# Kernel tuning notes

Measured on AMD Instinct MI355X. Metric: run time of the kernel, lower is better.

## Reference

```python
import jax, jax.numpy as jnp
import numpy as np

H, D, VD = 8, 64, 64
QD, KD, VDIM, OUT = 512, 512, 512, 512
N, QS, VS = 16, 512, 512
TEMP = 10.0              # softstair_temp
SCALING = D ** -0.5


def _softstair(x):
    fl = jnp.floor(x)
    return fl + jax.nn.sigmoid(TEMP * (jnp.abs(x - fl) - 0.5))


def setup_inputs() -> dict:
    key = jax.random.key(0)
    ks = jax.random.split(key, 24)
    f = jax.random.normal
    s = 0.03  # xavier-ish scale
    return {
        "Q": f(ks[0], (N, QS, QD), jnp.float32),
        "K": f(ks[1], (N, VS, KD), jnp.float32),
        "V": f(ks[2], (N, VS, VDIM), jnp.float32),
        "past_state": f(ks[3], (N, H, QS, D), jnp.float32),
        "past_attention": jax.random.uniform(ks[4], (N, H, QS, 1), jnp.float32),
        "value_positions": jnp.arange(VS, dtype=jnp.float32),
        "attention_mask": jnp.ones((N, QS, VS), jnp.int32),
        "Wq": f(ks[5], (QD, H * D), jnp.float32) * s,
        "Wk": f(ks[6], (KD, H * D), jnp.float32) * s,
        "Wv": f(ks[7], (VDIM, H * VD), jnp.float32) * s,
        "Wpos": f(ks[8], (QD, H * D), jnp.float32) * s,
        "bpos": f(ks[9], (H * D,), jnp.float32) * s,
        "Wsigma": f(ks[10], (H, D, 1), jnp.float32) * s,
        "Wrho": f(ks[11], (H, D, 3), jnp.float32) * s,
        "mix_w": f(ks[12], (QD, 1), jnp.float32) * s,
        "mix_b": f(ks[13], (1,), jnp.float32) * s,
        "gru_wi": f(ks[14], (D, 3 * D), jnp.float32) * s,
        "gru_wh": f(ks[15], (D, 3 * D), jnp.float32) * s,
        "gru_bi": f(ks[16], (3 * D,), jnp.float32) * s,
        "gru_bh": f(ks[17], (3 * D,), jnp.float32) * s,
        "Wc": f(ks[18], (H * VD, OUT), jnp.float32) * s,
    }


def reference(Q, K, V, past_state, past_attention, value_positions, attention_mask,
              Wq, Wk, Wv, Wpos, bpos, Wsigma, Wrho, mix_w, mix_b,
              gru_wi, gru_wh, gru_bi, gru_bh, Wc):
    n, qS, _ = Q.shape
    vS = K.shape[1]
    mask_f = attention_mask.astype(jnp.float32)          # [N,qS,vS]
    mask_b = attention_mask.astype(bool)[:, None]        # [N,1,qS,vS]
    lengths = jnp.sum(mask_f, axis=-1)                   # [N,qS]
    l_1 = jnp.maximum(1.0, lengths - 1.0)[:, None, :, None]
    step_size = 1.0 / l_1                                # [N,1,qS,1]
    nvp = value_positions[None, None, None, :] * step_size  # [N,1,qS,vS]

    # mix gate
    mix = jax.nn.sigmoid(Q @ mix_w + mix_b)[:, None]     # [N,1,qS,1]

    # projections -> [N,H,S,d]
    Qpos = (Q @ Wpos + bpos).reshape(n, qS, H, D).transpose(0, 2, 1, 3)
    Qh = (Q @ Wq).reshape(n, qS, H, D).transpose(0, 2, 1, 3)
    Kh = (K @ Wk).reshape(n, vS, H, D).transpose(0, 2, 1, 3)
    Vh = (V @ Wv).reshape(n, vS, H, VD).transpose(0, 2, 1, 3)

    # content attention
    content = jnp.einsum('bhqd,bhkd->bhqk', Qh, Kh) * SCALING
    content_attn = jax.nn.softmax(jnp.where(mask_b, content, -jnp.inf), axis=-1)

    # GRUCell update (torch gate order r,z,n) on relu(Qpos) with past_state
    x = jax.nn.relu(Qpos)
    gi = x @ gru_wi + gru_bi
    gh = past_state @ gru_wh + gru_bh
    ir, iz, inn = jnp.split(gi, 3, axis=-1)
    hr, hz, hn = jnp.split(gh, 3, axis=-1)
    r = jax.nn.sigmoid(ir + hr)
    z = jax.nn.sigmoid(iz + hz)
    nn_ = jnp.tanh(inn + r * hn)
    state = (1.0 - z) * nn_ + z * past_state             # [N,H,qS,D]

    # location (Gaussian) attention
    sigma = (jax.nn.relu(jnp.einsum('bhqd,hde->bhqe', state, Wsigma)) + 0.27) \
            / lengths[:, None, :, None]                  # [N,H,qS,1]
    rho = jnp.einsum('bhqd,hde->bhqe', state, Wrho)      # [N,H,qS,3]
    steps = _softstair(rho[..., 0:1])
    attn_gate = jax.nn.sigmoid(rho[..., 1:2])
    bias_gate = jax.nn.sigmoid(rho[..., 2:3])
    mu_ = steps * step_size + attn_gate * past_attention + bias_gate
    # leaky clamp to [0,1]
    mu = jnp.maximum(0.01 * mu_, jnp.minimum(mu_, 1.0 + 0.01 * mu_))
    diff = nvp - mu                                      # [N,H,qS,vS]
    gauss = jnp.exp(-(diff * diff) / (2.0 * sigma * sigma))
    g = gauss * mask_f[:, None]
    pos_attn = g / jnp.sum(g + 1e-20, axis=-1, keepdims=True)

    scores = mix * pos_attn + (1.0 - mix) * content_attn
    attended = jnp.einsum('bhqk,bhkv->bhqv', scores, Vh)
    out = attended.transpose(0, 2, 1, 3).reshape(n, qS, H * VD) @ Wc
    return out
```

## Files before the change

kernel.cpp:

```cpp
#include <hip/hip_runtime.h>


typedef __bf16 bf16;
typedef __bf16 bfx8 __attribute__((ext_vector_type(8)));
typedef float v4f __attribute__((ext_vector_type(4)));

__device__ inline float sigm(float x) { return 1.0f / (1.0f + __expf(-x)); }
__device__ inline float tanh_fast(float x) { return 1.0f - 2.0f / (__expf(2.0f * x) + 1.0f); }

__device__ inline v4f mfma16(bfx8 a, bfx8 b, v4f c) {
    return __builtin_amdgcn_mfma_f32_16x16x32_bf16(a, b, c, 0, 0, 0);
}

typedef const __attribute__((address_space(1))) void* gvp;
typedef __attribute__((address_space(3))) void* lvp;

__device__ inline void gload_lds16(const bf16* g, bf16* l) {
    __builtin_amdgcn_global_load_lds((gvp)g, (lvp)l, 16, 0, 0);
}

__device__ inline void split8(const float* __restrict__ p, bfx8& hi, bfx8& lo) {
    float4 x = *(const float4*)p;
    float4 y = *(const float4*)(p + 4);
    float v[8] = {x.x, x.y, x.z, x.w, y.x, y.y, y.z, y.w};
#pragma unroll
    for (int j = 0; j < 8; ++j) {
        bf16 h = (bf16)v[j];
        hi[j] = h;
        lo[j] = (bf16)(v[j] - (float)h);
    }
}

struct PrepArgs {
    const float* wsrc[5]; bf16* wdst[5]; bf16* wdstlo[5];
    const float* gwi; const float* gwh;
    bf16* wih; bf16* wil; bf16* whh; bf16* whl;
    const float* Q; const int* mask; const float* mix_w; const float* mix_b;
    float* mixv; float* stepv; float* lenv; unsigned* mpack;
};

__global__ __launch_bounds__(256) void prep_kernel(PrepArgs a) {
    __shared__ __align__(16) char smraw[17408];
    const int b = blockIdx.x;
    const int t = threadIdx.x;

    if (b < 320) {
        float (*tile)[68] = (float(*)[68])smraw;
        const int wy = b >> 6, bx = b & 63;
        const float* src = a.wsrc[wy];
        bf16* dst = a.wdst[wy];
        bf16* dlo = a.wdstlo[wy];
        const int rbase = (bx >> 3) * 64, cbase = (bx & 7) * 64;
        const int r = t >> 2, cc = (t & 3) * 16;
        {
            const float* p = src + (long)(rbase + r) * 512 + cbase + cc;
            *(float4*)(&tile[r][cc]) = *(const float4*)p;
            *(float4*)(&tile[r][cc + 4]) = *(const float4*)(p + 4);
            *(float4*)(&tile[r][cc + 8]) = *(const float4*)(p + 8);
            *(float4*)(&tile[r][cc + 12]) = *(const float4*)(p + 12);
        }
        __syncthreads();
        bfx8 h0, h1, l0, l1;
#pragma unroll
        for (int j = 0; j < 8; ++j) {
            float v0 = tile[cc + j][r];
            float v1 = tile[cc + 8 + j][r];
            bf16 a0 = (bf16)v0, a1 = (bf16)v1;
            h0[j] = a0; l0[j] = (bf16)(v0 - (float)a0);
            h1[j] = a1; l1[j] = (bf16)(v1 - (float)a1);
        }
        const int n_ = cbase + r;
        const int x_ = (n_ & 7) << 3;
        const long rowo = (long)n_ * 512;
        const int ka = (rbase + cc) ^ x_;
        const int kb = (rbase + cc + 8) ^ x_;
        *(bfx8*)(dst + rowo + ka) = h0;
        *(bfx8*)(dst + rowo + kb) = h1;
        if (dlo) {
            *(bfx8*)(dlo + rowo + ka) = l0;
            *(bfx8*)(dlo + rowo + kb) = l1;
        }
        return;
    }

    if (b < 322) {
        const int m = b - 320;
        const float* src = m ? a.gwh : a.gwi;
        bf16* dh = m ? a.whh : a.wih;
        bf16* dl = m ? a.whl : a.wil;
        for (int e = t; e < 12288; e += 256) {
            int row = e >> 7, col = e & 127;
            int cc = col >> 3, j = col & 7;
            int nt = row >> 3, ks = (row >> 2) & 1, quad = row & 3;
            int k = ks * 32 + quad * 8 + j;
            float v = src[k * 192 + nt * 16 + cc];
            bf16 h = (bf16)v;
            dh[e] = h;
            dl[e] = (bf16)(v - (float)h);
        }
        return;
    }

    unsigned (*mwords)[16] = (unsigned(*)[16])smraw;
    const int bm = b - 322;
    const int qt = bm & 31, n = bm >> 5;
    const int wave = t >> 6, lane = t & 63;
#pragma unroll
    for (int rr = 0; rr < 4; ++rr) {
        const int rloc = wave * 4 + rr;
        const long row = (long)n * 512 + qt * 16 + rloc;
        float dot = 0.f, ms = 0.f;
        unsigned myw = 0;
#pragma unroll
        for (int j = 0; j < 8; ++j) {
            float qv = a.Q[row * 512 + j * 64 + lane];
            float wv = a.mix_w[j * 64 + lane];
            dot += qv * wv;
            int mv = a.mask[row * 512 + j * 64 + lane];
            unsigned long long bl = __ballot(mv != 0);
            ms += (float)__popcll(bl);
            if ((lane >> 1) == j) myw = (unsigned)(bl >> ((lane & 1) * 32));
        }
#pragma unroll
        for (int o = 32; o > 0; o >>= 1) dot += __shfl_xor(dot, o);
        if (lane < 16) mwords[rloc][lane] = myw;
        if (lane == 0) {
            a.mixv[row] = sigm(dot + a.mix_b[0]);
            a.lenv[row] = ms;
            a.stepv[row] = 1.0f / fmaxf(1.0f, ms - 1.0f);
        }
    }
    __syncthreads();
    {
        const int quad = (lane >> 4), c = lane & 15;
        unsigned out = 0;
#pragma unroll
        for (int i = 0; i < 4; ++i) {
            const int rl = quad * 4 + i;
            unsigned w0 = mwords[rl][wave * 4 + 0];
            unsigned w1 = mwords[rl][wave * 4 + 1];
            unsigned w2 = mwords[rl][wave * 4 + 2];
            unsigned w3 = mwords[rl][wave * 4 + 3];
            unsigned byte_ = ((w0 >> c) & 1u) | (((w0 >> (16 + c)) & 1u) << 1) |
                             (((w1 >> c) & 1u) << 2) | (((w1 >> (16 + c)) & 1u) << 3) |
                             (((w2 >> c) & 1u) << 4) | (((w2 >> (16 + c)) & 1u) << 5) |
                             (((w3 >> c) & 1u) << 6) | (((w3 >> (16 + c)) & 1u) << 7);
            out |= byte_ << (8 * i);
        }
        a.mpack[(long)bm * 256 + t] = out;
    }
}

struct GEMMDesc {
    const float* Af;
    const bf16* Ab;
    const bf16* B0;
    const bf16* B1;
    const float* bias;
    bf16* Cb;
    bf16* Cl;
    float* Cf;
    int mode;
    float cscale;
};
struct G4 { GEMMDesc d[4]; };

__global__ __launch_bounds__(256, 2) void gemm128(G4 gg) {
    __shared__ bf16 sm[32768];

    const GEMMDesc g = gg.d[blockIdx.z];
    const int mode = g.mode;
    const int mbase = blockIdx.x * 128, nbase = blockIdx.y * 128;
    const int t = threadIdx.x, w = t >> 6, l = t & 63;
    const int quad = l >> 4, c = l & 15;
    const int wr = w >> 1, wc = w & 1;

    const v4f zero4 = {0.f, 0.f, 0.f, 0.f};
    v4f acc[4][4];
#pragma unroll
    for (int m = 0; m < 4; ++m)
#pragma unroll
        for (int nn = 0; nn < 4; ++nn) acc[m][nn] = zero4;

    const int nsteps = (mode == 2) ? 24 : 8;
    const int arow_t = t >> 3;
    const int ach = t & 7;
    const int asw = ((ach ^ (arow_t & 7)) * 8);
    const int xm = c & 7;
    const int slot0 = w * 4;
    const int srow = l >> 3;
    const int sch8 = (l & 7) * 8;

    float4 ax[4], ay[4];

    auto issue = [&](int s, bf16* As, bf16* Bs) {
        const bf16* Bsrc = g.B0;
        int k0;
        if (mode == 2) {
            int ph = s >> 3;
            k0 = (s & 7) * 64;
            if (ph == 1) Bsrc = g.B1;
        } else {
            k0 = s * 64;
        }
#pragma unroll
        for (int j = 0; j < 4; ++j) {
            int sl = slot0 + j;
            int row = sl * 8 + srow;
            gload_lds16(Bsrc + (long)(nbase + row) * 512 + k0 + sch8, Bs + sl * 512);
        }
        if (mode == 3) {
#pragma unroll
            for (int j = 0; j < 4; ++j) {
                int sl = slot0 + j;
                int row = sl * 8 + srow;
                gload_lds16(g.Ab + (long)(mbase + row) * 512 + k0 + sch8, As + sl * 512);
            }
        } else {
#pragma unroll
            for (int j = 0; j < 4; ++j) {
                const float* p = g.Af + (long)(mbase + j * 32 + arow_t) * 512 + k0 + ach * 8;
                ax[j] = *(const float4*)p;
                ay[j] = *(const float4*)(p + 4);
            }
        }
    };

    auto writeA = [&](int s, bf16* As) {
        if (mode == 3) return;
        const bool lo = (mode == 2) && ((s >> 3) == 2);
#pragma unroll
        for (int j = 0; j < 4; ++j) {
            float v[8] = {ax[j].x, ax[j].y, ax[j].z, ax[j].w,
                          ay[j].x, ay[j].y, ay[j].z, ay[j].w};
            bfx8 hv;
            if (!lo) {
#pragma unroll
                for (int q = 0; q < 8; ++q) hv[q] = (bf16)v[q];
            } else {
#pragma unroll
                for (int q = 0; q < 8; ++q) {
                    bf16 h = (bf16)v[q];
                    hv[q] = (bf16)(v[q] - (float)h);
                }
            }
            *(bfx8*)(&As[(j * 32 + arow_t) * 64 + asw]) = hv;
        }
    };

    auto compute = [&](const bf16* As, const bf16* Bs) {
#pragma unroll
        for (int ks = 0; ks < 2; ++ks) {
            const int off = (((ks * 4 + quad) ^ xm) * 8);
            bfx8 af[4], bb[4];
#pragma unroll
            for (int m = 0; m < 4; ++m)
                af[m] = *(const bfx8*)(&As[(wr * 64 + m * 16 + c) * 64 + off]);
#pragma unroll
            for (int nn = 0; nn < 4; ++nn)
                bb[nn] = *(const bfx8*)(&Bs[(wc * 64 + nn * 16 + c) * 64 + off]);
#pragma unroll
            for (int m = 0; m < 4; ++m)
#pragma unroll
                for (int nn = 0; nn < 4; ++nn)
                    acc[m][nn] = mfma16(af[m], bb[nn], acc[m][nn]);
        }
    };

    issue(0, sm, sm + 8192);
    writeA(0, sm);
    __syncthreads();
    for (int s = 0; s < nsteps; ++s) {
        bf16* Ac = sm + (s & 1) * 16384;
        bf16* An = sm + (((s & 1) ^ 1) * 16384);
        const bool more = (s + 1 < nsteps);
        if (more) issue(s + 1, An, An + 8192);
        compute(Ac, Ac + 8192);
        if (more) writeA(s + 1, An);
        __syncthreads();
    }

    if (mode == 3) {
        float* C = g.Cf;
#pragma unroll
        for (int m = 0; m < 4; ++m)
#pragma unroll
            for (int nn = 0; nn < 4; ++nn)
#pragma unroll
                for (int i = 0; i < 4; ++i) {
                    int row = mbase + wr * 64 + m * 16 + quad * 4 + i;
                    int col = nbase + wc * 64 + nn * 16 + c;
                    C[(long)row * 512 + col] = acc[m][nn][i];
                }
        return;
    }

    if (mode == 1) {
        bf16* CT = g.Cb + ((long)(mbase >> 9)) * 262144;
        const int s0 = mbase & 511;
        for (int h = 0; h < 2; ++h) {
            if (wr == h) {
#pragma unroll
                for (int m = 0; m < 4; ++m)
#pragma unroll
                    for (int nn = 0; nn < 4; ++nn)
#pragma unroll
                        for (int i = 0; i < 4; ++i)
                            sm[(wc * 64 + nn * 16 + c) * 64 + m * 16 + quad * 4 + i] =
                                (bf16)acc[m][nn][i];
            }
            __syncthreads();
            {
                const bf16* src = sm + (t >> 1) * 64 + (t & 1) * 32;
                bf16* d = CT + (long)(nbase + (t >> 1)) * 512 + s0 + h * 64 + (t & 1) * 32;
#pragma unroll
                for (int j = 0; j < 4; ++j) *(bfx8*)(d + j * 8) = *(const bfx8*)(src + j * 8);
            }
            __syncthreads();
        }
        return;
    }

    for (int h = 0; h < 2; ++h) {
        if (wr == h) {
#pragma unroll
            for (int m = 0; m < 4; ++m)
#pragma unroll
                for (int nn = 0; nn < 4; ++nn)
#pragma unroll
                    for (int i = 0; i < 4; ++i) {
                        int col = wc * 64 + nn * 16 + c;
                        float v = acc[m][nn][i];
                        if (mode == 2) v = fmaxf(v + g.bias[nbase + col], 0.f);
                        else v *= g.cscale;
                        bf16 hv = (bf16)v;
                        sm[(m * 16 + quad * 4 + i) * 128 + col] = hv;
                        if (mode == 2)
                            sm[8192 + (m * 16 + quad * 4 + i) * 128 + col] =
                                (bf16)(v - (float)hv);
                    }
        }
        __syncthreads();
        {
            const int row = t >> 2, seg = t & 3;
            const bf16* src = sm + row * 128 + seg * 32;
            bf16* d = g.Cb + (long)(mbase + h * 64 + row) * 512 + nbase + seg * 32;
#pragma unroll
            for (int j = 0; j < 4; ++j) *(bfx8*)(d + j * 8) = *(const bfx8*)(src + j * 8);
            if (mode == 2) {
                const bf16* src2 = sm + 8192 + row * 128 + seg * 32;
                bf16* d2 = g.Cl + (long)(mbase + h * 64 + row) * 512 + nbase + seg * 32;
#pragma unroll
                for (int j = 0; j < 4; ++j) *(bfx8*)(d2 + j * 8) = *(const bfx8*)(src2 + j * 8);
            }
        }
        __syncthreads();
    }
}

__global__ __launch_bounds__(256) void gru_fused_kernel(
    const bf16* __restrict__ Xh, const bf16* __restrict__ Xl,
    const float* __restrict__ hp,
    const bf16* __restrict__ wih, const bf16* __restrict__ wil,
    const bf16* __restrict__ whh, const bf16* __restrict__ whl,
    const float* __restrict__ gbi, const float* __restrict__ gbh,
    const float* __restrict__ pa, const float* __restrict__ Wsigma,
    const float* __restrict__ Wrho,
    const float* __restrict__ lenv, const float* __restrict__ stepv,
    float* __restrict__ muv, float* __restrict__ sigv) {
    const int b = blockIdx.x;
    const int qb = b & 7, nh = b >> 3, hd = nh & 7, n = nh >> 3;
    const int t = threadIdx.x;
    const int w = t >> 6, lane = t & 63, quad = lane >> 4, c = lane & 15;
    const int q0 = qb * 64 + w * 16;
    const int fbase = quad * 128 + c * 8;

    const v4f zero4 = {0.f, 0.f, 0.f, 0.f};
    v4f gi[12], gh[12];
#pragma unroll
    for (int nt = 0; nt < 12; ++nt) gi[nt] = zero4;
#pragma unroll
    for (int ks = 0; ks < 2; ++ks) {
        long ao = (long)(n * 512 + q0 + c) * 512 + hd * 64 + ks * 32 + quad * 8;
        bfx8 xh = *(const bfx8*)(Xh + ao);
        bfx8 xl = *(const bfx8*)(Xl + ao);
#pragma unroll
        for (int nt = 0; nt < 12; ++nt) {
            const int fo = (nt * 2 + ks) * 512 + fbase;
            bfx8 bh = *(const bfx8*)(wih + fo);
            bfx8 bl = *(const bfx8*)(wil + fo);
            gi[nt] = mfma16(xh, bh, gi[nt]);
            gi[nt] = mfma16(xh, bl, gi[nt]);
            gi[nt] = mfma16(xl, bh, gi[nt]);
        }
    }
#pragma unroll
    for (int nt = 0; nt < 12; ++nt) gh[nt] = zero4;
#pragma unroll
    for (int ks = 0; ks < 2; ++ks) {
        bfx8 ah, al;
        split8(hp + (long)(nh * 512 + q0 + c) * 64 + ks * 32 + quad * 8, ah, al);
#pragma unroll
        for (int nt = 0; nt < 12; ++nt) {
            const int fo = (nt * 2 + ks) * 512 + fbase;
            bfx8 bh = *(const bfx8*)(whh + fo);
            bfx8 bl = *(const bfx8*)(whl + fo);
            gh[nt] = mfma16(ah, bh, gh[nt]);
            gh[nt] = mfma16(ah, bl, gh[nt]);
            gh[nt] = mfma16(al, bh, gh[nt]);
        }
    }

    float st[4][4];
#pragma unroll
    for (int t4 = 0; t4 < 4; ++t4) {
        float bir = gbi[t4 * 16 + c];
        float biz = gbi[64 + t4 * 16 + c];
        float bin = gbi[128 + t4 * 16 + c];
        float bhr = gbh[t4 * 16 + c];
        float bhz = gbh[64 + t4 * 16 + c];
        float bhn = gbh[128 + t4 * 16 + c];
#pragma unroll
        for (int i = 0; i < 4; ++i) {
            int row = q0 + quad * 4 + i;
            float r = sigm(gi[t4][i] + bir + gh[t4][i] + bhr);
            float z = sigm(gi[t4 + 4][i] + biz + gh[t4 + 4][i] + bhz);
            float nn_ = tanh_fast(gi[t4 + 8][i] + bin + r * (gh[t4 + 8][i] + bhn));
            float hpv = hp[(long)(nh * 512 + row) * 64 + t4 * 16 + c];
            st[t4][i] = (1.0f - z) * nn_ + z * hpv;
        }
    }

    float ws_[4], wr0[4], wr1[4], wr2[4];
#pragma unroll
    for (int t4 = 0; t4 < 4; ++t4) {
        int d = t4 * 16 + c;
        ws_[t4] = Wsigma[hd * 64 + d];
        wr0[t4] = Wrho[(hd * 64 + d) * 3 + 0];
        wr1[t4] = Wrho[(hd * 64 + d) * 3 + 1];
        wr2[t4] = Wrho[(hd * 64 + d) * 3 + 2];
    }
#pragma unroll
    for (int i = 0; i < 4; ++i) {
        float s0 = 0.f, s1 = 0.f, s2 = 0.f, s3 = 0.f;
#pragma unroll
        for (int t4 = 0; t4 < 4; ++t4) {
            float sv = st[t4][i];
            s0 += sv * ws_[t4];
            s1 += sv * wr0[t4];
            s2 += sv * wr1[t4];
            s3 += sv * wr2[t4];
        }
#pragma unroll
        for (int o = 1; o < 16; o <<= 1) {
            s0 += __shfl_xor(s0, o);
            s1 += __shfl_xor(s1, o);
            s2 += __shfl_xor(s2, o);
            s3 += __shfl_xor(s3, o);
        }
        if (c == 0) {
            int row = q0 + quad * 4 + i;
            int idx = nh * 512 + row, rq = n * 512 + row;
            float L = lenv[rq], sp = stepv[rq];
            float sg = (fmaxf(s0, 0.f) + 0.27f) / L;
            float fl = floorf(s1);
            float steps = fl + sigm(10.0f * (fabsf(s1 - fl) - 0.5f));
            float ag = sigm(s2), bg = sigm(s3);
            float mu_ = steps * sp + ag * pa[idx] + bg;
            float mu = fmaxf(0.01f * mu_, fminf(mu_, 1.0f + 0.01f * mu_));
            muv[idx] = mu;
            sigv[idx] = sg;
        }
    }
}

__global__ __launch_bounds__(256) void attn_fused_kernel(
    const bf16* __restrict__ Qh, const bf16* __restrict__ Kh,
    const bf16* __restrict__ VhT, const unsigned* __restrict__ mpack,
    const float* __restrict__ vpos, const float* __restrict__ mixv,
    const float* __restrict__ stepv, const float* __restrict__ muv,
    const float* __restrict__ sigv, bf16* __restrict__ att) {
    __shared__ bf16 Pp[16][520];
    __shared__ bf16 Pg[16][520];

    const int b = blockIdx.x;
    const int nh = ((b >> 8) << 3) | (b & 7);
    const int qt = (b >> 3) & 31;
    const int hd = nh & 7, n = nh >> 3;
    const int t = threadIdx.x;
    const int wave = t >> 6, lane = t & 63;
    const int quad = lane >> 4, c = lane & 15;
    const int qloc = quad * 4;

    const bf16* qrow = Qh + (long)(n * 512 + qt * 16 + c) * 512 + hd * 64 + quad * 8;
    bfx8 afr0 = *(const bfx8*)qrow;
    bfx8 afr1 = *(const bfx8*)(qrow + 32);

    const v4f zero4 = {0.f, 0.f, 0.f, 0.f};
    v4f acc[8];
#pragma unroll
    for (int i = 0; i < 8; ++i) acc[i] = zero4;

    const bf16* kbase = Kh + (long)(n * 512 + wave * 128 + c) * 512 + hd * 64 + quad * 8;
#pragma unroll
    for (int t8 = 0; t8 < 8; ++t8) {
        bfx8 b0 = *(const bfx8*)(kbase + (long)t8 * 16 * 512);
        bfx8 b1 = *(const bfx8*)(kbase + (long)t8 * 16 * 512 + 32);
        acc[t8] = mfma16(afr0, b0, acc[t8]);
        acc[t8] = mfma16(afr1, b1, acc[t8]);
    }

    float mu_[4], c2n[4], stp[4];
#pragma unroll
    for (int i = 0; i < 4; ++i) {
        int q = qt * 16 + qloc + i;
        int idx = nh * 512 + q, rq = n * 512 + q;
        mu_[i] = muv[idx];
        float sg = sigv[idx];
        c2n[i] = -0.72134752f / (sg * sg);
        stp[i] = stepv[rq];
    }

    const unsigned mb32 = mpack[(long)(n * 32 + qt) * 256 + t];
    unsigned mbits[4];
#pragma unroll
    for (int i = 0; i < 4; ++i) mbits[i] = (mb32 >> (8 * i)) & 0xffu;

    float vp[8];
#pragma unroll
    for (int t8 = 0; t8 < 8; ++t8) vp[t8] = vpos[wave * 128 + t8 * 16 + c];

#pragma unroll
    for (int i = 0; i < 4; ++i) {
        float m = mu_[i], s = stp[i], cg = c2n[i];
#pragma unroll
        for (int t8 = 0; t8 < 8; ++t8) {
            int on = (mbits[i] >> t8) & 1;
            float pv = on ? __builtin_amdgcn_exp2f(acc[t8][i]) : 0.f;
            float d = vp[t8] * s - m;
            float gv = on ? __builtin_amdgcn_exp2f(d * d * cg) : 0.f;
            int k = wave * 128 + t8 * 16 + c;
            Pp[qloc + i][k] = (bf16)pv;
            Pg[qloc + i][k] = (bf16)gv;
        }
    }

    __syncthreads();

    bfx8 ones;
#pragma unroll
    for (int j = 0; j < 8; ++j) ones[j] = (bf16)1.0f;

    v4f accP = zero4, accG = zero4, accS = zero4, accT = zero4;
    const bf16* vrow = VhT + (long)(n * 512 + hd * 64 + wave * 16 + c) * 512 + quad * 8;
    __builtin_amdgcn_s_setprio(1);
#pragma unroll
    for (int ks = 0; ks < 16; ++ks) {
        bfx8 bf_ = *(const bfx8*)(vrow + ks * 32);
        bfx8 ap = *(const bfx8*)(&Pp[c][ks * 32 + quad * 8]);
        bfx8 ag = *(const bfx8*)(&Pg[c][ks * 32 + quad * 8]);
        accP = mfma16(ap, bf_, accP);
        accG = mfma16(ag, bf_, accG);
        accS = mfma16(ap, ones, accS);
        accT = mfma16(ag, ones, accT);
    }
    __builtin_amdgcn_s_setprio(0);

#pragma unroll
    for (int i = 0; i < 4; ++i) {
        float Sp = accS[i];
        float Sg = accT[i] + 512.0f * 1e-20f;
        float m_ = mixv[n * 512 + qt * 16 + qloc + i];
        float aci = (1.0f - m_) / Sp;
        float bci = m_ / Sg;
        int q = qt * 16 + quad * 4 + i;
        int cx = (wave * 16 + c) ^ (((quad * 4 + i) & 7) << 3);
        att[(long)(n * 512 + q) * 512 + hd * 64 + cx] =
            (bf16)(aci * accP[i] + bci * accG[i]);
    }
}

extern "C" void kernel_launch(void* const* d_in, const int* in_sizes, int n_in,
                              void* d_out, int out_size, void* d_ws, size_t ws_size,
                              hipStream_t stream) {
    (void)in_sizes; (void)n_in; (void)out_size; (void)ws_size;

    const float* Q = (const float*)d_in[0];
    const float* K = (const float*)d_in[1];
    const float* V = (const float*)d_in[2];
    const float* past_state = (const float*)d_in[3];
    const float* past_att = (const float*)d_in[4];
    const float* vpos = (const float*)d_in[5];
    const int* mask = (const int*)d_in[6];
    const float* Wq = (const float*)d_in[7];
    const float* Wk = (const float*)d_in[8];
    const float* Wv = (const float*)d_in[9];
    const float* Wpos = (const float*)d_in[10];
    const float* bpos = (const float*)d_in[11];
    const float* Wsigma = (const float*)d_in[12];
    const float* Wrho = (const float*)d_in[13];
    const float* mix_w = (const float*)d_in[14];
    const float* mix_b = (const float*)d_in[15];
    const float* gwi = (const float*)d_in[16];
    const float* gwh = (const float*)d_in[17];
    const float* gbi = (const float*)d_in[18];
    const float* gbh = (const float*)d_in[19];
    const float* Wc = (const float*)d_in[20];
    float* out = (float*)d_out;

    char* p = (char*)d_ws;
    const size_t SZB = 8192UL * 512 * 2;
    const size_t SZW = 512UL * 512 * 2;
    bf16* WqT = (bf16*)p;   p += SZW;
    bf16* WkT = (bf16*)p;   p += SZW;
    bf16* WvT = (bf16*)p;   p += SZW;
    bf16* WpT = (bf16*)p;   p += SZW;
    bf16* WpTl = (bf16*)p;  p += SZW;
    bf16* WcT = (bf16*)p;   p += SZW;
    bf16* wih = (bf16*)p;   p += 24576;
    bf16* wil = (bf16*)p;   p += 24576;
    bf16* whh = (bf16*)p;   p += 24576;
    bf16* whl = (bf16*)p;   p += 24576;
    bf16* Qh = (bf16*)p;    p += SZB;
    bf16* Kh = (bf16*)p;    p += SZB;
    bf16* VhT = (bf16*)p;   p += SZB;
    bf16* Xh = (bf16*)p;
    bf16* att = Xh;         p += SZB;
    bf16* Xl = (bf16*)p;    p += SZB;
    unsigned* mpack = (unsigned*)p;      p += 16UL * 32 * 256 * 4;
    float* mixv = (float*)p;  p += 32768;
    float* stepv = (float*)p; p += 32768;
    float* lenv = (float*)p;  p += 32768;
    float* muv = (float*)p;   p += 262144;
    float* sigv = (float*)p;  p += 262144;

    dim3 blk(256);

    PrepArgs pa;
    pa.wsrc[0] = Wq; pa.wsrc[1] = Wk; pa.wsrc[2] = Wv; pa.wsrc[3] = Wpos; pa.wsrc[4] = Wc;
    pa.wdst[0] = WqT; pa.wdst[1] = WkT; pa.wdst[2] = WvT; pa.wdst[3] = WpT; pa.wdst[4] = WcT;
    pa.wdstlo[0] = nullptr; pa.wdstlo[1] = nullptr; pa.wdstlo[2] = nullptr;
    pa.wdstlo[3] = WpTl; pa.wdstlo[4] = nullptr;
    pa.gwi = gwi; pa.gwh = gwh;
    pa.wih = wih; pa.wil = wil; pa.whh = whh; pa.whl = whl;
    pa.Q = Q; pa.mask = mask; pa.mix_w = mix_w; pa.mix_b = mix_b;
    pa.mixv = mixv; pa.stepv = stepv; pa.lenv = lenv; pa.mpack = mpack;
    prep_kernel<<<dim3(834), blk, 0, stream>>>(pa);

    G4 gp;
    gp.d[0].Af = Q;  gp.d[0].Ab = nullptr; gp.d[0].B0 = WpT; gp.d[0].B1 = WpTl;
    gp.d[0].bias = bpos; gp.d[0].Cb = Xh; gp.d[0].Cl = Xl; gp.d[0].Cf = nullptr;
    gp.d[0].mode = 2; gp.d[0].cscale = 1.0f;
    gp.d[1].Af = Q;  gp.d[1].Ab = nullptr; gp.d[1].B0 = WqT; gp.d[1].B1 = nullptr;
    gp.d[1].bias = nullptr; gp.d[1].Cb = Qh; gp.d[1].Cl = nullptr; gp.d[1].Cf = nullptr;
    gp.d[1].mode = 0; gp.d[1].cscale = 0.125f * 1.44269504089f;
    gp.d[2].Af = K;  gp.d[2].Ab = nullptr; gp.d[2].B0 = WkT; gp.d[2].B1 = nullptr;
    gp.d[2].bias = nullptr; gp.d[2].Cb = Kh; gp.d[2].Cl = nullptr; gp.d[2].Cf = nullptr;
    gp.d[2].mode = 0; gp.d[2].cscale = 1.0f;
    gp.d[3].Af = V;  gp.d[3].Ab = nullptr; gp.d[3].B0 = WvT; gp.d[3].B1 = nullptr;
    gp.d[3].bias = nullptr; gp.d[3].Cb = VhT; gp.d[3].Cl = nullptr; gp.d[3].Cf = nullptr;
    gp.d[3].mode = 1; gp.d[3].cscale = 1.0f;
    gemm128<<<dim3(64, 4, 4), blk, 0, stream>>>(gp);

    gru_fused_kernel<<<dim3(1024), blk, 0, stream>>>(
        Xh, Xl, past_state, wih, wil, whh, whl, gbi, gbh, past_att, Wsigma, Wrho,
        lenv, stepv, muv, sigv);

    attn_fused_kernel<<<dim3(4096), blk, 0, stream>>>(
        Qh, Kh, VhT, mpack, vpos, mixv, stepv, muv, sigv, att);

    G4 go;
    go.d[0].Af = nullptr; go.d[0].Ab = att; go.d[0].B0 = WcT; go.d[0].B1 = nullptr;
    go.d[0].bias = nullptr; go.d[0].Cb = nullptr; go.d[0].Cl = nullptr; go.d[0].Cf = out;
    go.d[0].mode = 3; go.d[0].cscale = 1.0f;
    go.d[1] = go.d[0]; go.d[2] = go.d[0]; go.d[3] = go.d[0];
    gemm128<<<dim3(64, 4, 1), blk, 0, stream>>>(go);
}
```

Before: 338.3 us.

## Pre-convert Q/K/V to bf16 in prep and load GEMM A operands directly to registers

The prep kernel gains extra blocks that convert Q, K and V from fp32 to bf16, plus a low-order split of Q, into new workspace buffers. The projection GEMM then reads A fragments straight from global memory into registers instead of staging converted fp32 through LDS, which halves shared memory and raises launch bounds to 3 blocks per SU. The GRU kernel stages its weights and biases in LDS with a plain row layout, and the attention output drops its XOR swizzle. The cost is an extra full pass over Q/K/V in memory and uncoalesced register loads of A, in exchange for less LDS traffic and higher occupancy in the GEMM.

```diff
diff --git a/kernel.cpp b/kernel.cpp
--- a/kernel.cpp
+++ b/kernel.cpp
@@ -37,6 +37,8 @@
     bf16* wih; bf16* wil; bf16* whh; bf16* whl;
     const float* Q; const int* mask; const float* mix_w; const float* mix_b;
     float* mixv; float* stepv; float* lenv; unsigned* mpack;
+    const float* Kf; const float* Vf;
+    bf16* Qbf; bf16* Qlo; bf16* Kbf; bf16* Vbf;
 };
 
 __global__ __launch_bounds__(256) void prep_kernel(PrepArgs a) {
@@ -89,11 +91,8 @@
         bf16* dh = m ? a.whh : a.wih;
         bf16* dl = m ? a.whl : a.wil;
         for (int e = t; e < 12288; e += 256) {
-            int row = e >> 7, col = e & 127;
-            int cc = col >> 3, j = col & 7;
-            int nt = row >> 3, ks = (row >> 2) & 1, quad = row & 3;
-            int k = ks * 32 + quad * 8 + j;
-            float v = src[k * 192 + nt * 16 + cc];
+            int n_ = e >> 6, k = e & 63;
+            float v = src[k * 192 + n_];
             bf16 h = (bf16)v;
             dh[e] = h;
             dl[e] = (bf16)(v - (float)h);
@@ -101,59 +100,86 @@
         return;
     }
 
-    unsigned (*mwords)[16] = (unsigned(*)[16])smraw;
-    const int bm = b - 322;
-    const int qt = bm & 31, n = bm >> 5;
-    const int wave = t >> 6, lane = t & 63;
-#pragma unroll
-    for (int rr = 0; rr < 4; ++rr) {
-        const int rloc = wave * 4 + rr;
-        const long row = (long)n * 512 + qt * 16 + rloc;
-        float dot = 0.f, ms = 0.f;
-        unsigned myw = 0;
-#pragma unroll
-        for (int j = 0; j < 8; ++j) {
-            float qv = a.Q[row * 512 + j * 64 + lane];
-            float wv = a.mix_w[j * 64 + lane];
-            dot += qv * wv;
-            int mv = a.mask[row * 512 + j * 64 + lane];
-            unsigned long long bl = __ballot(mv != 0);
-            ms += (float)__popcll(bl);
-            if ((lane >> 1) == j) myw = (unsigned)(bl >> ((lane & 1) * 32));
-        }
-#pragma unroll
-        for (int o = 32; o > 0; o >>= 1) dot += __shfl_xor(dot, o);
-        if (lane < 16) mwords[rloc][lane] = myw;
-        if (lane == 0) {
-            a.mixv[row] = sigm(dot + a.mix_b[0]);
-            a.lenv[row] = ms;
-            a.stepv[row] = 1.0f / fmaxf(1.0f, ms - 1.0f);
-        }
-    }
-    __syncthreads();
-    {
-        const int quad = (lane >> 4), c = lane & 15;
-        unsigned out = 0;
-#pragma unroll
-        for (int i = 0; i < 4; ++i) {
-            const int rl = quad * 4 + i;
-            unsigned w0 = mwords[rl][wave * 4 + 0];
-            unsigned w1 = mwords[rl][wave * 4 + 1];
-            unsigned w2 = mwords[rl][wave * 4 + 2];
-            unsigned w3 = mwords[rl][wave * 4 + 3];
-            unsigned byte_ = ((w0 >> c) & 1u) | (((w0 >> (16 + c)) & 1u) << 1) |
-                             (((w1 >> c) & 1u) << 2) | (((w1 >> (16 + c)) & 1u) << 3) |
-                             (((w2 >> c) & 1u) << 4) | (((w2 >> (16 + c)) & 1u) << 5) |
-                             (((w3 >> c) & 1u) << 6) | (((w3 >> (16 + c)) & 1u) << 7);
-            out |= byte_ << (8 * i);
-        }
-        a.mpack[(long)bm * 256 + t] = out;
+    if (b < 834) {
+        unsigned (*mwords)[16] = (unsigned(*)[16])smraw;
+        const int bm = b - 322;
+        const int qt = bm & 31, n = bm >> 5;
+        const int wave = t >> 6, lane = t & 63;
+#pragma unroll
+        for (int rr = 0; rr < 4; ++rr) {
+            const int rloc = wave * 4 + rr;
+            const long row = (long)n * 512 + qt * 16 + rloc;
+            float dot = 0.f, ms = 0.f;
+            unsigned myw = 0;
+#pragma unroll
+            for (int j = 0; j < 8; ++j) {
+                float qv = a.Q[row * 512 + j * 64 + lane];
+                float wv = a.mix_w[j * 64 + lane];
+                dot += qv * wv;
+                int mv = a.mask[row * 512 + j * 64 + lane];
+                unsigned long long bl = __ballot(mv != 0);
+                ms += (float)__popcll(bl);
+                if ((lane >> 1) == j) myw = (unsigned)(bl >> ((lane & 1) * 32));
+            }
+#pragma unroll
+            for (int o = 32; o > 0; o >>= 1) dot += __shfl_xor(dot, o);
+            if (lane < 16) mwords[rloc][lane] = myw;
+            if (lane == 0) {
+                a.mixv[row] = sigm(dot + a.mix_b[0]);
+                a.lenv[row] = ms;
+                a.stepv[row] = 1.0f / fmaxf(1.0f, ms - 1.0f);
+            }
+        }
+        __syncthreads();
+        {
+            const int quad = (lane >> 4), c = lane & 15;
+            unsigned out = 0;
+#pragma unroll
+            for (int i = 0; i < 4; ++i) {
+                const int rl = quad * 4 + i;
+                unsigned w0 = mwords[rl][wave * 4 + 0];
+                unsigned w1 = mwords[rl][wave * 4 + 1];
+                unsigned w2 = mwords[rl][wave * 4 + 2];
+                unsigned w3 = mwords[rl][wave * 4 + 3];
+                unsigned byte_ = ((w0 >> c) & 1u) | (((w0 >> (16 + c)) & 1u) << 1) |
+                                 (((w1 >> c) & 1u) << 2) | (((w1 >> (16 + c)) & 1u) << 3) |
+                                 (((w2 >> c) & 1u) << 4) | (((w2 >> (16 + c)) & 1u) << 5) |
+                                 (((w3 >> c) & 1u) << 6) | (((w3 >> (16 + c)) & 1u) << 7);
+                out |= byte_ << (8 * i);
+            }
+            a.mpack[(long)bm * 256 + t] = out;
+        }
+        return;
+    }
+
+    const int cb = b - 834;
+    const int tensor = cb >> 10;
+    const long off = ((long)(cb & 1023) * 256 + t) * 16;
+    const float* s_ = tensor == 0 ? a.Q : (tensor == 1 ? a.Kf : a.Vf);
+    const float4* sp = (const float4*)(s_ + off);
+    float4 x0 = sp[0], x1 = sp[1], x2 = sp[2], x3 = sp[3];
+    float v[16] = {x0.x, x0.y, x0.z, x0.w, x1.x, x1.y, x1.z, x1.w,
+                   x2.x, x2.y, x2.z, x2.w, x3.x, x3.y, x3.z, x3.w};
+    bfx8 h0, h1, l0, l1;
+#pragma unroll
+    for (int j = 0; j < 8; ++j) {
+        bf16 ha = (bf16)v[j], hb = (bf16)v[8 + j];
+        h0[j] = ha; h1[j] = hb;
+        l0[j] = (bf16)(v[j] - (float)ha);
+        l1[j] = (bf16)(v[8 + j] - (float)hb);
+    }
+    bf16* dh = tensor == 0 ? a.Qbf : (tensor == 1 ? a.Kbf : a.Vbf);
+    *(bfx8*)(dh + off) = h0;
+    *(bfx8*)(dh + off + 8) = h1;
+    if (tensor == 0) {
+        *(bfx8*)(a.Qlo + off) = l0;
+        *(bfx8*)(a.Qlo + off + 8) = l1;
     }
 }
 
 struct GEMMDesc {
-    const float* Af;
-    const bf16* Ab;
+    const bf16* A0;
+    const bf16* A1;
     const bf16* B0;
     const bf16* B1;
     const float* bias;
@@ -165,8 +191,10 @@
 };
 struct G4 { GEMMDesc d[4]; };
 
-__global__ __launch_bounds__(256, 2) void gemm128(G4 gg) {
-    __shared__ bf16 sm[32768];
+__global__ __launch_bounds__(256, 3) void gemm128(G4 gg) {
+    __shared__ bf16 sm[16384];
+    bf16* Bs0 = sm;
+    bf16* Bs1 = sm + 8192;
 
     const GEMMDesc g = gg.d[blockIdx.z];
     const int mode = g.mode;
@@ -183,79 +211,39 @@
         for (int nn = 0; nn < 4; ++nn) acc[m][nn] = zero4;
 
     const int nsteps = (mode == 2) ? 24 : 8;
-    const int arow_t = t >> 3;
-    const int ach = t & 7;
-    const int asw = ((ach ^ (arow_t & 7)) * 8);
     const int xm = c & 7;
     const int slot0 = w * 4;
     const int srow = l >> 3;
     const int sch8 = (l & 7) * 8;
-
-    float4 ax[4], ay[4];
-
-    auto issue = [&](int s, bf16* As, bf16* Bs) {
-        const bf16* Bsrc = g.B0;
-        int k0;
-        if (mode == 2) {
-            int ph = s >> 3;
-            k0 = (s & 7) * 64;
-            if (ph == 1) Bsrc = g.B1;
-        } else {
-            k0 = s * 64;
-        }
+    const long arow = (long)(mbase + wr * 64 + c) * 512 + quad * 8;
+
+    auto issueB = [&](int s, bf16* Bs) {
+        const bf16* Bsrc = (mode == 2 && ((s >> 3) == 1)) ? g.B1 : g.B0;
+        const int k0 = (mode == 2) ? (s & 7) * 64 : s * 64;
 #pragma unroll
         for (int j = 0; j < 4; ++j) {
             int sl = slot0 + j;
             int row = sl * 8 + srow;
             gload_lds16(Bsrc + (long)(nbase + row) * 512 + k0 + sch8, Bs + sl * 512);
         }
-        if (mode == 3) {
-#pragma unroll
-            for (int j = 0; j < 4; ++j) {
-                int sl = slot0 + j;
-                int row = sl * 8 + srow;
-                gload_lds16(g.Ab + (long)(mbase + row) * 512 + k0 + sch8, As + sl * 512);
-            }
-        } else {
-#pragma unroll
-            for (int j = 0; j < 4; ++j) {
-                const float* p = g.Af + (long)(mbase + j * 32 + arow_t) * 512 + k0 + ach * 8;
-                ax[j] = *(const float4*)p;
-                ay[j] = *(const float4*)(p + 4);
-            }
-        }
     };
 
-    auto writeA = [&](int s, bf16* As) {
-        if (mode == 3) return;
-        const bool lo = (mode == 2) && ((s >> 3) == 2);
-#pragma unroll
-        for (int j = 0; j < 4; ++j) {
-            float v[8] = {ax[j].x, ax[j].y, ax[j].z, ax[j].w,
-                          ay[j].x, ay[j].y, ay[j].z, ay[j].w};
-            bfx8 hv;
-            if (!lo) {
-#pragma unroll
-                for (int q = 0; q < 8; ++q) hv[q] = (bf16)v[q];
-            } else {
-#pragma unroll
-                for (int q = 0; q < 8; ++q) {
-                    bf16 h = (bf16)v[q];
-                    hv[q] = (bf16)(v[q] - (float)h);
-                }
-            }
-            *(bfx8*)(&As[(j * 32 + arow_t) * 64 + asw]) = hv;
+    auto loadA = [&](int s, bfx8 (&dst)[8]) {
+        const bf16* Asrc = (mode == 2 && ((s >> 3) == 2)) ? g.A1 : g.A0;
+        const int k0 = (mode == 2) ? (s & 7) * 64 : s * 64;
+#pragma unroll
+        for (int m = 0; m < 4; ++m) {
+            const bf16* pr = Asrc + arow + (long)m * 16 * 512 + k0;
+            dst[m * 2 + 0] = *(const bfx8*)pr;
+            dst[m * 2 + 1] = *(const bfx8*)(pr + 32);
         }
     };
 
-    auto compute = [&](const bf16* As, const bf16* Bs) {
+    auto computeB = [&](const bf16* Bs, const bfx8 (&af)[8]) {
 #pragma unroll
         for (int ks = 0; ks < 2; ++ks) {
             const int off = (((ks * 4 + quad) ^ xm) * 8);
-            bfx8 af[4], bb[4];
-#pragma unroll
-            for (int m = 0; m < 4; ++m)
-                af[m] = *(const bfx8*)(&As[(wr * 64 + m * 16 + c) * 64 + off]);
+            bfx8 bb[4];
 #pragma unroll
             for (int nn = 0; nn < 4; ++nn)
                 bb[nn] = *(const bfx8*)(&Bs[(wc * 64 + nn * 16 + c) * 64 + off]);
@@ -263,20 +251,25 @@
             for (int m = 0; m < 4; ++m)
 #pragma unroll
                 for (int nn = 0; nn < 4; ++nn)
-                    acc[m][nn] = mfma16(af[m], bb[nn], acc[m][nn]);
+                    acc[m][nn] = mfma16(af[m * 2 + ks], bb[nn], acc[m][nn]);
         }
     };
 
-    issue(0, sm, sm + 8192);
-    writeA(0, sm);
+    bfx8 aA[8], aB[8];
+    issueB(0, Bs0);
+    loadA(0, aA);
     __syncthreads();
-    for (int s = 0; s < nsteps; ++s) {
-        bf16* Ac = sm + (s & 1) * 16384;
-        bf16* An = sm + (((s & 1) ^ 1) * 16384);
-        const bool more = (s + 1 < nsteps);
-        if (more) issue(s + 1, An, An + 8192);
-        compute(Ac, Ac + 8192);
-        if (more) writeA(s + 1, An);
+    for (int s = 0; s < nsteps; s += 2) {
+        issueB(s + 1, Bs1);
+        loadA(s + 1, aB);
+        computeB(Bs0, aA);
+        __syncthreads();
+        const bool more = (s + 2 < nsteps);
+        if (more) {
+            issueB(s + 2, Bs0);
+            loadA(s + 2, aA);
+        }
+        computeB(Bs1, aB);
         __syncthreads();
     }
 
@@ -368,12 +361,24 @@
     const float* __restrict__ Wrho,
     const float* __restrict__ lenv, const float* __restrict__ stepv,
     float* __restrict__ muv, float* __restrict__ sigv) {
+    __shared__ bf16 Wh[192][72], Wl[192][72];
+    __shared__ float biL[384];
+
     const int b = blockIdx.x;
     const int qb = b & 7, nh = b >> 3, hd = nh & 7, n = nh >> 3;
     const int t = threadIdx.x;
     const int w = t >> 6, lane = t & 63, quad = lane >> 4, c = lane & 15;
     const int q0 = qb * 64 + w * 16;
-    const int fbase = quad * 128 + c * 8;
+
+    if (t < 192) { biL[t] = gbi[t]; biL[192 + t] = gbh[t]; }
+#pragma unroll
+    for (int it = 0; it < 6; ++it) {
+        int task = it * 256 + t;
+        int r = task >> 3, ch = task & 7;
+        *(bfx8*)(&Wh[r][ch * 8]) = *(const bfx8*)(wih + r * 64 + ch * 8);
+        *(bfx8*)(&Wl[r][ch * 8]) = *(const bfx8*)(wil + r * 64 + ch * 8);
+    }
+    __syncthreads();
 
     const v4f zero4 = {0.f, 0.f, 0.f, 0.f};
     v4f gi[12], gh[12];
@@ -386,14 +391,22 @@
         bfx8 xl = *(const bfx8*)(Xl + ao);
 #pragma unroll
         for (int nt = 0; nt < 12; ++nt) {
-            const int fo = (nt * 2 + ks) * 512 + fbase;
-            bfx8 bh = *(const bfx8*)(wih + fo);
-            bfx8 bl = *(const bfx8*)(wil + fo);
+            bfx8 bh = *(const bfx8*)(&Wh[nt * 16 + c][ks * 32 + quad * 8]);
+            bfx8 bl = *(const bfx8*)(&Wl[nt * 16 + c][ks * 32 + quad * 8]);
             gi[nt] = mfma16(xh, bh, gi[nt]);
             gi[nt] = mfma16(xh, bl, gi[nt]);
             gi[nt] = mfma16(xl, bh, gi[nt]);
         }
     }
+    __syncthreads();
+#pragma unroll
+    for (int it = 0; it < 6; ++it) {
+        int task = it * 256 + t;
+        int r = task >> 3, ch = task & 7;
+        *(bfx8*)(&Wh[r][ch * 8]) = *(const bfx8*)(whh + r * 64 + ch * 8);
+        *(bfx8*)(&Wl[r][ch * 8]) = *(const bfx8*)(whl + r * 64 + ch * 8);
+    }
+    __syncthreads();
 #pragma unroll
     for (int nt = 0; nt < 12; ++nt) gh[nt] = zero4;
 #pragma unroll
@@ -402,9 +415,8 @@
         split8(hp + (long)(nh * 512 + q0 + c) * 64 + ks * 32 + quad * 8, ah, al);
 #pragma unroll
         for (int nt = 0; nt < 12; ++nt) {
-            const int fo = (nt * 2 + ks) * 512 + fbase;
-            bfx8 bh = *(const bfx8*)(whh + fo);
-            bfx8 bl = *(const bfx8*)(whl + fo);
+            bfx8 bh = *(const bfx8*)(&Wh[nt * 16 + c][ks * 32 + quad * 8]);
+            bfx8 bl = *(const bfx8*)(&Wl[nt * 16 + c][ks * 32 + quad * 8]);
             gh[nt] = mfma16(ah, bh, gh[nt]);
             gh[nt] = mfma16(ah, bl, gh[nt]);
             gh[nt] = mfma16(al, bh, gh[nt]);
@@ -414,12 +426,12 @@
     float st[4][4];
 #pragma unroll
     for (int t4 = 0; t4 < 4; ++t4) {
-        float bir = gbi[t4 * 16 + c];
-        float biz = gbi[64 + t4 * 16 + c];
-        float bin = gbi[128 + t4 * 16 + c];
-        float bhr = gbh[t4 * 16 + c];
-        float bhz = gbh[64 + t4 * 16 + c];
-        float bhn = gbh[128 + t4 * 16 + c];
+        float bir = biL[t4 * 16 + c];
+        float biz = biL[64 + t4 * 16 + c];
+        float bin = biL[128 + t4 * 16 + c];
+        float bhr = biL[192 + t4 * 16 + c];
+        float bhz = biL[256 + t4 * 16 + c];
+        float bhn = biL[320 + t4 * 16 + c];
 #pragma unroll
         for (int i = 0; i < 4; ++i) {
             int row = q0 + quad * 4 + i;
@@ -574,8 +586,7 @@
         float aci = (1.0f - m_) / Sp;
         float bci = m_ / Sg;
         int q = qt * 16 + quad * 4 + i;
-        int cx = (wave * 16 + c) ^ (((quad * 4 + i) & 7) << 3);
-        att[(long)(n * 512 + q) * 512 + hd * 64 + cx] =
+        att[(long)(n * 512 + q) * 512 + hd * 64 + wave * 16 + c] =
             (bf16)(aci * accP[i] + bci * accG[i]);
     }
 }
@@ -627,6 +638,10 @@
     bf16* Xh = (bf16*)p;
     bf16* att = Xh;         p += SZB;
     bf16* Xl = (bf16*)p;    p += SZB;
+    bf16* Qbf = (bf16*)p;   p += SZB;
+    bf16* Qlo = (bf16*)p;   p += SZB;
+    bf16* Kbf = (bf16*)p;   p += SZB;
+    bf16* Vbf = (bf16*)p;   p += SZB;
     unsigned* mpack = (unsigned*)p;      p += 16UL * 32 * 256 * 4;
     float* mixv = (float*)p;  p += 32768;
     float* stepv = (float*)p; p += 32768;
@@ -645,19 +660,21 @@
     pa.wih = wih; pa.wil = wil; pa.whh = whh; pa.whl = whl;
     pa.Q = Q; pa.mask = mask; pa.mix_w = mix_w; pa.mix_b = mix_b;
     pa.mixv = mixv; pa.stepv = stepv; pa.lenv = lenv; pa.mpack = mpack;
-    prep_kernel<<<dim3(834), blk, 0, stream>>>(pa);
+    pa.Kf = K; pa.Vf = V;
+    pa.Qbf = Qbf; pa.Qlo = Qlo; pa.Kbf = Kbf; pa.Vbf = Vbf;
+    prep_kernel<<<dim3(3906), blk, 0, stream>>>(pa);
 
     G4 gp;
-    gp.d[0].Af = Q;  gp.d[0].Ab = nullptr; gp.d[0].B0 = WpT; gp.d[0].B1 = WpTl;
+    gp.d[0].A0 = Qbf; gp.d[0].A1 = Qlo; gp.d[0].B0 = WpT; gp.d[0].B1 = WpTl;
     gp.d[0].bias = bpos; gp.d[0].Cb = Xh; gp.d[0].Cl = Xl; gp.d[0].Cf = nullptr;
     gp.d[0].mode = 2; gp.d[0].cscale = 1.0f;
-    gp.d[1].Af = Q;  gp.d[1].Ab = nullptr; gp.d[1].B0 = WqT; gp.d[1].B1 = nullptr;
+    gp.d[1].A0 = Qbf; gp.d[1].A1 = nullptr; gp.d[1].B0 = WqT; gp.d[1].B1 = nullptr;
     gp.d[1].bias = nullptr; gp.d[1].Cb = Qh; gp.d[1].Cl = nullptr; gp.d[1].Cf = nullptr;
     gp.d[1].mode = 0; gp.d[1].cscale = 0.125f * 1.44269504089f;
-    gp.d[2].Af = K;  gp.d[2].Ab = nullptr; gp.d[2].B0 = WkT; gp.d[2].B1 = nullptr;
+    gp.d[2].A0 = Kbf; gp.d[2].A1 = nullptr; gp.d[2].B0 = WkT; gp.d[2].B1 = nullptr;
     gp.d[2].bias = nullptr; gp.d[2].Cb = Kh; gp.d[2].Cl = nullptr; gp.d[2].Cf = nullptr;
     gp.d[2].mode = 0; gp.d[2].cscale = 1.0f;
-    gp.d[3].Af = V;  gp.d[3].Ab = nullptr; gp.d[3].B0 = WvT; gp.d[3].B1 = nullptr;
+    gp.d[3].A0 = Vbf; gp.d[3].A1 = nullptr; gp.d[3].B0 = WvT; gp.d[3].B1 = nullptr;
     gp.d[3].bias = nullptr; gp.d[3].Cb = VhT; gp.d[3].Cl = nullptr; gp.d[3].Cf = nullptr;
     gp.d[3].mode = 1; gp.d[3].cscale = 1.0f;
     gemm128<<<dim3(64, 4, 4), blk, 0, stream>>>(gp);
@@ -670,7 +687,7 @@
         Qh, Kh, VhT, mpack, vpos, mixv, stepv, muv, sigv, att);
 
     G4 go;
-    go.d[0].Af = nullptr; go.d[0].Ab = att; go.d[0].B0 = WcT; go.d[0].B1 = nullptr;
+    go.d[0].A0 = att; go.d[0].A1 = nullptr; go.d[0].B0 = WcT; go.d[0].B1 = nullptr;
     go.d[0].bias = nullptr; go.d[0].Cb = nullptr; go.d[0].Cl = nullptr; go.d[0].Cf = out;
     go.d[0].mode = 3; go.d[0].cscale = 1.0f;
     go.d[1] = go.d[0]; go.d[2] = go.d[0]; go.d[3] = go.d[0];
```

New measurement: 370.0 us. 1.09x slower.

## Stage GRU weights in LDS and XOR-swizzle attention probability buffers

Applied to the files above, without the earlier changes.

The GRU kernel now copies the input and hidden weight matrices (hi/lo bf16) and biases into shared memory once per block and reads the MFMA B fragments from there instead of re-reading global memory. The prep kernel stores these weights in plain row-major order to match. The attention kernel drops its padded P buffers in favour of an XOR swizzle to avoid LDS bank conflicts, which also shrinks LDS use, and sets a minimum-occupancy launch bound. The cost is extra syncs and LDS pressure in the GRU kernel, plus possible register spills from the occupancy hint.

```diff
diff --git a/kernel.cpp b/kernel.cpp
--- a/kernel.cpp
+++ b/kernel.cpp
@@ -89,11 +89,8 @@
         bf16* dh = m ? a.whh : a.wih;
         bf16* dl = m ? a.whl : a.wil;
         for (int e = t; e < 12288; e += 256) {
-            int row = e >> 7, col = e & 127;
-            int cc = col >> 3, j = col & 7;
-            int nt = row >> 3, ks = (row >> 2) & 1, quad = row & 3;
-            int k = ks * 32 + quad * 8 + j;
-            float v = src[k * 192 + nt * 16 + cc];
+            int n_ = e >> 6, k = e & 63;
+            float v = src[k * 192 + n_];
             bf16 h = (bf16)v;
             dh[e] = h;
             dl[e] = (bf16)(v - (float)h);
@@ -368,12 +365,24 @@
     const float* __restrict__ Wrho,
     const float* __restrict__ lenv, const float* __restrict__ stepv,
     float* __restrict__ muv, float* __restrict__ sigv) {
+    __shared__ bf16 Wh[192][72], Wl[192][72];
+    __shared__ float biL[384];
+
     const int b = blockIdx.x;
     const int qb = b & 7, nh = b >> 3, hd = nh & 7, n = nh >> 3;
     const int t = threadIdx.x;
     const int w = t >> 6, lane = t & 63, quad = lane >> 4, c = lane & 15;
     const int q0 = qb * 64 + w * 16;
-    const int fbase = quad * 128 + c * 8;
+
+    if (t < 192) { biL[t] = gbi[t]; biL[192 + t] = gbh[t]; }
+#pragma unroll
+    for (int it = 0; it < 6; ++it) {
+        int task = it * 256 + t;
+        int r = task >> 3, ch = task & 7;
+        *(bfx8*)(&Wh[r][ch * 8]) = *(const bfx8*)(wih + r * 64 + ch * 8);
+        *(bfx8*)(&Wl[r][ch * 8]) = *(const bfx8*)(wil + r * 64 + ch * 8);
+    }
+    __syncthreads();
 
     const v4f zero4 = {0.f, 0.f, 0.f, 0.f};
     v4f gi[12], gh[12];
@@ -386,14 +395,22 @@
         bfx8 xl = *(const bfx8*)(Xl + ao);
 #pragma unroll
         for (int nt = 0; nt < 12; ++nt) {
-            const int fo = (nt * 2 + ks) * 512 + fbase;
-            bfx8 bh = *(const bfx8*)(wih + fo);
-            bfx8 bl = *(const bfx8*)(wil + fo);
+            bfx8 bh = *(const bfx8*)(&Wh[nt * 16 + c][ks * 32 + quad * 8]);
+            bfx8 bl = *(const bfx8*)(&Wl[nt * 16 + c][ks * 32 + quad * 8]);
             gi[nt] = mfma16(xh, bh, gi[nt]);
             gi[nt] = mfma16(xh, bl, gi[nt]);
             gi[nt] = mfma16(xl, bh, gi[nt]);
         }
     }
+    __syncthreads();
+#pragma unroll
+    for (int it = 0; it < 6; ++it) {
+        int task = it * 256 + t;
+        int r = task >> 3, ch = task & 7;
+        *(bfx8*)(&Wh[r][ch * 8]) = *(const bfx8*)(whh + r * 64 + ch * 8);
+        *(bfx8*)(&Wl[r][ch * 8]) = *(const bfx8*)(whl + r * 64 + ch * 8);
+    }
+    __syncthreads();
 #pragma unroll
     for (int nt = 0; nt < 12; ++nt) gh[nt] = zero4;
 #pragma unroll
@@ -402,9 +419,8 @@
         split8(hp + (long)(nh * 512 + q0 + c) * 64 + ks * 32 + quad * 8, ah, al);
 #pragma unroll
         for (int nt = 0; nt < 12; ++nt) {
-            const int fo = (nt * 2 + ks) * 512 + fbase;
-            bfx8 bh = *(const bfx8*)(whh + fo);
-            bfx8 bl = *(const bfx8*)(whl + fo);
+            bfx8 bh = *(const bfx8*)(&Wh[nt * 16 + c][ks * 32 + quad * 8]);
+            bfx8 bl = *(const bfx8*)(&Wl[nt * 16 + c][ks * 32 + quad * 8]);
             gh[nt] = mfma16(ah, bh, gh[nt]);
             gh[nt] = mfma16(ah, bl, gh[nt]);
             gh[nt] = mfma16(al, bh, gh[nt]);
@@ -414,12 +430,12 @@
     float st[4][4];
 #pragma unroll
     for (int t4 = 0; t4 < 4; ++t4) {
-        float bir = gbi[t4 * 16 + c];
-        float biz = gbi[64 + t4 * 16 + c];
-        float bin = gbi[128 + t4 * 16 + c];
-        float bhr = gbh[t4 * 16 + c];
-        float bhz = gbh[64 + t4 * 16 + c];
-        float bhn = gbh[128 + t4 * 16 + c];
+        float bir = biL[t4 * 16 + c];
+        float biz = biL[64 + t4 * 16 + c];
+        float bin = biL[128 + t4 * 16 + c];
+        float bhr = biL[192 + t4 * 16 + c];
+        float bhz = biL[256 + t4 * 16 + c];
+        float bhn = biL[320 + t4 * 16 + c];
 #pragma unroll
         for (int i = 0; i < 4; ++i) {
             int row = q0 + quad * 4 + i;
@@ -474,14 +490,14 @@
     }
 }
 
-__global__ __launch_bounds__(256) void attn_fused_kernel(
+__global__ __launch_bounds__(256, 5) void attn_fused_kernel(
     const bf16* __restrict__ Qh, const bf16* __restrict__ Kh,
     const bf16* __restrict__ VhT, const unsigned* __restrict__ mpack,
     const float* __restrict__ vpos, const float* __restrict__ mixv,
     const float* __restrict__ stepv, const float* __restrict__ muv,
     const float* __restrict__ sigv, bf16* __restrict__ att) {
-    __shared__ bf16 Pp[16][520];
-    __shared__ bf16 Pg[16][520];
+    __shared__ bf16 Pp[16][512];
+    __shared__ bf16 Pg[16][512];
 
     const int b = blockIdx.x;
     const int nh = ((b >> 8) << 3) | (b & 7);
@@ -533,13 +549,14 @@
 #pragma unroll
     for (int i = 0; i < 4; ++i) {
         float m = mu_[i], s = stp[i], cg = c2n[i];
+        const int rsw = ((qloc + i) & 7) << 3;
 #pragma unroll
         for (int t8 = 0; t8 < 8; ++t8) {
             int on = (mbits[i] >> t8) & 1;
             float pv = on ? __builtin_amdgcn_exp2f(acc[t8][i]) : 0.f;
             float d = vp[t8] * s - m;
             float gv = on ? __builtin_amdgcn_exp2f(d * d * cg) : 0.f;
-            int k = wave * 128 + t8 * 16 + c;
+            int k = (wave * 128 + t8 * 16 + c) ^ rsw;
             Pp[qloc + i][k] = (bf16)pv;
             Pg[qloc + i][k] = (bf16)gv;
         }
@@ -553,12 +570,14 @@
 
     v4f accP = zero4, accG = zero4, accS = zero4, accT = zero4;
     const bf16* vrow = VhT + (long)(n * 512 + hd * 64 + wave * 16 + c) * 512 + quad * 8;
+    const int csw = (c & 7) << 3;
     __builtin_amdgcn_s_setprio(1);
 #pragma unroll
     for (int ks = 0; ks < 16; ++ks) {
         bfx8 bf_ = *(const bfx8*)(vrow + ks * 32);
-        bfx8 ap = *(const bfx8*)(&Pp[c][ks * 32 + quad * 8]);
-        bfx8 ag = *(const bfx8*)(&Pg[c][ks * 32 + quad * 8]);
+        const int kr = (ks * 32 + quad * 8) ^ csw;
+        bfx8 ap = *(const bfx8*)(&Pp[c][kr]);
+        bfx8 ag = *(const bfx8*)(&Pg[c][kr]);
         accP = mfma16(ap, bf_, accP);
         accG = mfma16(ag, bf_, accG);
         accS = mfma16(ap, ones, accS);
```

Result: faster. 323.3 us (-4.4%).
